# Performance work log

Hardware: AMD Instinct MI355X
Metric: run time of the kernel (lower is better)

The kernel has to match this reference:

```python
import jax, jax.numpy as jnp
import numpy as np
from jax import lax

G0, G1 = 16, 16
UNITS = 256


def setup_inputs() -> dict:
    key = jax.random.key(0)
    ks = jax.random.split(key, 20)
    B, H, W, C = 64, 512, 512, 3
    U = UNITS
    flat = 12 * 12 * 3  # after two VALID 3x3 convs on 16x16x3
    inp = {
        'image': jax.random.normal(ks[0], (B, H, W, C), jnp.float32),
        'section': jax.random.uniform(ks[1], (B, 3), jnp.float32),
        'h0': jax.random.normal(ks[2], (B, U), jnp.float32) * 0.1,
        'c0': jax.random.normal(ks[3], (B, U), jnp.float32) * 0.1,
        'conv1_k': jax.random.normal(ks[4], (3, 3, C, 3), jnp.float32) * 0.2,
        'conv1_b': jnp.zeros((3,), jnp.float32),
        'conv2_k': jax.random.normal(ks[5], (3, 3, 3, 3), jnp.float32) * 0.2,
        'conv2_b': jnp.zeros((3,), jnp.float32),
        'dense_w': jax.random.normal(ks[6], (flat, U), jnp.float32) * (1.0 / np.sqrt(flat)),
        'dense_b': jnp.zeros((U,), jnp.float32),
        'lstm_k': jax.random.normal(ks[7], (U, 4 * U), jnp.float32) * (1.0 / np.sqrt(U)),
        'lstm_rk': jax.random.normal(ks[8], (U, 4 * U), jnp.float32) * (1.0 / np.sqrt(U)),
        'lstm_b': jnp.zeros((4 * U,), jnp.float32),
        'nsc_w1': jax.random.normal(ks[9], (U, U), jnp.float32) * (1.0 / np.sqrt(U)),
        'nsc_b1': jnp.zeros((U,), jnp.float32),
        'nsc_w2': jax.random.normal(ks[10], (U, 3), jnp.float32) * (1.0 / np.sqrt(U)),
        'nsc_b2': jnp.zeros((3,), jnp.float32),
    }
    return inp


def _interpolate(image, section):
    # image: (B,H,W,C); section: (B,3) = (x, y, scale); coords in [0,1],
    # mapped linearly onto grid indices with constant (clamp) extension,
    # matching tfp.math.batch_interp_regular_nd_grid over image axes 1,2.
    B, H, W, C = image.shape
    starts = section[:, :2]                       # (B,2)
    stops = section[:, :2] + section[:, 2:]       # (B,2) broadcast scale
    t0 = jnp.linspace(0.0, 1.0, G0)               # along grid_dim[0]
    alpha = jnp.linspace(0.0, 1.0, G1)            # along grid_dim[1]
    # p0[b,i,j]: coordinate mapped to image axis 1 (H)
    p0 = (starts[:, 0, None] + t0[None, :] * (stops[:, 0] - starts[:, 0])[:, None])[:, :, None]
    p0 = jnp.broadcast_to(p0, (B, G0, G1))
    # p1[b,i,j]: coordinate mapped to image axis 2 (W)
    p1 = (starts[:, 1, None] + alpha[None, :] * (stops[:, 1] - starts[:, 1])[:, None])[:, None, :]
    p1 = jnp.broadcast_to(p1, (B, G0, G1))
    fy = jnp.clip(p0 * (H - 1), 0.0, H - 1)
    fx = jnp.clip(p1 * (W - 1), 0.0, W - 1)
    y0 = jnp.floor(fy).astype(jnp.int32)
    x0 = jnp.floor(fx).astype(jnp.int32)
    y1 = jnp.minimum(y0 + 1, H - 1)
    x1 = jnp.minimum(x0 + 1, W - 1)
    wy = (fy - y0)[..., None]
    wx = (fx - x0)[..., None]
    b = jnp.arange(B)[:, None, None]
    v00 = image[b, y0, x0]
    v01 = image[b, y0, x1]
    v10 = image[b, y1, x0]
    v11 = image[b, y1, x1]
    top = v00 * (1 - wx) + v01 * wx
    bot = v10 * (1 - wx) + v11 * wx
    return top * (1 - wy) + bot * wy            # (B,G0,G1,C)


def _conv_relu(x, k, b):
    y = lax.conv_general_dilated(x, k, (1, 1), 'VALID',
                                 dimension_numbers=('NHWC', 'HWIO', 'NHWC'))
    return jax.nn.relu(y + b)


def reference(image, section, h0, c0, conv1_k, conv1_b, conv2_k, conv2_b,
              dense_w, dense_b, lstm_k, lstm_rk, lstm_b,
              nsc_w1, nsc_b1, nsc_w2, nsc_b2):
    sec = _interpolate(image, section)                 # (B,16,16,C)
    x = _conv_relu(sec, conv1_k, conv1_b)              # (B,14,14,3)
    x = _conv_relu(x, conv2_k, conv2_b)                # (B,12,12,3)
    x = x.reshape(x.shape[0], -1)                      # (B,432)
    x = jax.nn.relu(x @ dense_w + dense_b)             # (B,U)
    # Keras LSTMCell: gate order i, f, g(c), o
    z = x @ lstm_k + h0 @ lstm_rk + lstm_b
    i, f, g, o = jnp.split(z, 4, axis=-1)
    c_new = jax.nn.sigmoid(f) * c0 + jax.nn.sigmoid(i) * jnp.tanh(g)
    h_new = jax.nn.sigmoid(o) * jnp.tanh(c_new)
    nsc = jax.nn.relu(h_new @ nsc_w1 + nsc_b1)
    next_section = jax.nn.sigmoid(nsc @ nsc_w2 + nsc_b2)  # (B,3)
    return h_new, c_new, next_section
```

## Files before the change

kernel.cpp:

```cpp
#include <hip/hip_runtime.h>
#include <math.h>

#define BATCH 64
#define IMH 512
#define IMW 512
#define UNITS 256

__device__ __forceinline__ float sigmoidf_(float x) {
    return 1.0f / (1.0f + __expf(-x));
}
__device__ __forceinline__ float tanhf_(float x) {
    float e = __expf(2.0f * x);
    return 1.0f - 2.0f / (e + 1.0f);
}

__global__ __launch_bounds__(1024) void fused_cell_kernel(
    const float* __restrict__ image,
    const float* __restrict__ section,
    const float* __restrict__ h0,
    const float* __restrict__ c0,
    const float* __restrict__ k1,
    const float* __restrict__ b1,
    const float* __restrict__ k2,
    const float* __restrict__ b2,
    const float* __restrict__ dw,
    const float* __restrict__ db,
    const float* __restrict__ lk,
    const float* __restrict__ lrk,
    const float* __restrict__ lb,
    const float* __restrict__ w1,
    const float* __restrict__ nb1,
    const float* __restrict__ w2,
    const float* __restrict__ nb2,
    float* __restrict__ out)
{
    const int b   = blockIdx.x;
    const int tid = threadIdx.x;

    __shared__ float s_sec[16][16][3];
    __shared__ float s_c1[14][14][3];
    __shared__ float s_flat[432];
    __shared__ float s_x[256];
    __shared__ float s_h0[256];
    __shared__ float s_hn[256];
    __shared__ float s_nsc[256];
    __shared__ float s_z[1024];
    __shared__ float s_part[4][256];
    __shared__ float s_k1[84];
    __shared__ float s_k2[84];

    if (tid < 81)       s_k1[tid]      = k1[tid];
    else if (tid < 84)  s_k1[tid]      = b1[tid - 81];
    else if (tid < 165) s_k2[tid - 84] = k2[tid - 84];
    else if (tid < 168) s_k2[tid - 84] = b2[tid - 165];
    if (tid < 256) s_h0[tid] = h0[b * UNITS + tid];

    if (tid < 256) {
        const float s0 = section[b * 3 + 0];
        const float s1 = section[b * 3 + 1];
        const float s2 = section[b * 3 + 2];
        const int i = tid >> 4, j = tid & 15;
        float p0 = s0 + (float)i * (1.0f / 15.0f) * s2;
        float p1 = s1 + (float)j * (1.0f / 15.0f) * s2;
        float fy = fminf(fmaxf(p0 * 511.0f, 0.0f), 511.0f);
        float fx = fminf(fmaxf(p1 * 511.0f, 0.0f), 511.0f);
        int y0 = (int)floorf(fy);
        int x0 = (int)floorf(fx);
        int y1 = min(y0 + 1, 511);
        int x1 = min(x0 + 1, 511);
        float wy = fy - (float)y0;
        float wx = fx - (float)x0;
        const float* base = image + (size_t)b * IMH * IMW * 3;
        const float* p00 = base + (y0 * IMW + x0) * 3;
        const float* p01 = base + (y0 * IMW + x1) * 3;
        const float* p10 = base + (y1 * IMW + x0) * 3;
        const float* p11 = base + (y1 * IMW + x1) * 3;
        #pragma unroll
        for (int c = 0; c < 3; ++c) {
            float top = p00[c] * (1.0f - wx) + p01[c] * wx;
            float bot = p10[c] * (1.0f - wx) + p11[c] * wx;
            s_sec[i][j][c] = top * (1.0f - wy) + bot * wy;
        }
    }
    __syncthreads();

    if (tid < 196) {
        const int i = tid / 14, j = tid % 14;
        float a0 = s_k1[81], a1 = s_k1[82], a2 = s_k1[83];
        #pragma unroll
        for (int di = 0; di < 3; ++di)
            #pragma unroll
            for (int dj = 0; dj < 3; ++dj)
                #pragma unroll
                for (int ci = 0; ci < 3; ++ci) {
                    float v = s_sec[i + di][j + dj][ci];
                    const int kb = ((di * 3 + dj) * 3 + ci) * 3;
                    a0 += v * s_k1[kb + 0];
                    a1 += v * s_k1[kb + 1];
                    a2 += v * s_k1[kb + 2];
                }
        s_c1[i][j][0] = fmaxf(a0, 0.0f);
        s_c1[i][j][1] = fmaxf(a1, 0.0f);
        s_c1[i][j][2] = fmaxf(a2, 0.0f);
    }
    __syncthreads();

    if (tid < 144) {
        const int i = tid / 12, j = tid % 12;
        float a0 = s_k2[81], a1 = s_k2[82], a2 = s_k2[83];
        #pragma unroll
        for (int di = 0; di < 3; ++di)
            #pragma unroll
            for (int dj = 0; dj < 3; ++dj)
                #pragma unroll
                for (int ci = 0; ci < 3; ++ci) {
                    float v = s_c1[i + di][j + dj][ci];
                    const int kb = ((di * 3 + dj) * 3 + ci) * 3;
                    a0 += v * s_k2[kb + 0];
                    a1 += v * s_k2[kb + 1];
                    a2 += v * s_k2[kb + 2];
                }
        const int fb = tid * 3;
        s_flat[fb + 0] = fmaxf(a0, 0.0f);
        s_flat[fb + 1] = fmaxf(a1, 0.0f);
        s_flat[fb + 2] = fmaxf(a2, 0.0f);
    }
    __syncthreads();

    {
        const int g = tid >> 8, col = tid & 255;
        const float* wp = dw + (g * 108) * 256 + col;
        const float* fp = s_flat + g * 108;
        float acc = 0.0f;
        #pragma unroll 6
        for (int k = 0; k < 108; ++k)
            acc += fp[k] * wp[k * 256];
        s_part[g][col] = acc;
    }
    __syncthreads();
    if (tid < 256)
        s_x[tid] = fmaxf(s_part[0][tid] + s_part[1][tid] + s_part[2][tid] +
                         s_part[3][tid] + db[tid], 0.0f);
    __syncthreads();

    {
        float z = lb[tid];
        const float* lkp = lk  + tid;
        const float* lrp = lrk + tid;
        #pragma unroll 8
        for (int k = 0; k < 256; ++k)
            z += s_x[k] * lkp[k * 1024] + s_h0[k] * lrp[k * 1024];
        s_z[tid] = z;
    }
    __syncthreads();
    if (tid < 256) {
        const float zi = s_z[tid];
        const float zf = s_z[256 + tid];
        const float zg = s_z[512 + tid];
        const float zo = s_z[768 + tid];
        const float cprev = c0[b * UNITS + tid];
        const float cn = sigmoidf_(zf) * cprev + sigmoidf_(zi) * tanhf_(zg);
        const float hn = sigmoidf_(zo) * tanhf_(cn);
        out[b * UNITS + tid] = hn;
        out[BATCH * UNITS + b * UNITS + tid] = cn;
        s_hn[tid] = hn;
    }
    __syncthreads();

    {
        const int g = tid >> 8, col = tid & 255;
        const float* wp = w1 + (g * 64) * 256 + col;
        const float* hp = s_hn + g * 64;
        float acc = 0.0f;
        #pragma unroll 8
        for (int k = 0; k < 64; ++k)
            acc += hp[k] * wp[k * 256];
        s_part[g][col] = acc;
    }
    __syncthreads();
    if (tid < 256)
        s_nsc[tid] = fmaxf(s_part[0][tid] + s_part[1][tid] + s_part[2][tid] +
                           s_part[3][tid] + nb1[tid], 0.0f);
    __syncthreads();

    if (tid < 192) {
        const int j = tid >> 6;
        const int l = tid & 63;
        float p = 0.0f;
        #pragma unroll
        for (int k = l; k < 256; k += 64)
            p += s_nsc[k] * w2[k * 3 + j];
        #pragma unroll
        for (int off = 32; off > 0; off >>= 1)
            p += __shfl_down(p, off);
        if (l == 0)
            out[2 * BATCH * UNITS + b * 3 + j] = sigmoidf_(p + nb2[j]);
    }
}

extern "C" void kernel_launch(void* const* d_in, const int* in_sizes, int n_in,
                              void* d_out, int out_size, void* d_ws, size_t ws_size,
                              hipStream_t stream) {
    const float* image   = (const float*)d_in[0];
    const float* section = (const float*)d_in[1];
    const float* h0      = (const float*)d_in[2];
    const float* c0      = (const float*)d_in[3];
    const float* k1      = (const float*)d_in[4];
    const float* b1      = (const float*)d_in[5];
    const float* k2      = (const float*)d_in[6];
    const float* b2      = (const float*)d_in[7];
    const float* dw      = (const float*)d_in[8];
    const float* db      = (const float*)d_in[9];
    const float* lk      = (const float*)d_in[10];
    const float* lrk     = (const float*)d_in[11];
    const float* lb      = (const float*)d_in[12];
    const float* w1      = (const float*)d_in[13];
    const float* nb1     = (const float*)d_in[14];
    const float* w2      = (const float*)d_in[15];
    const float* nb2     = (const float*)d_in[16];
    float* out = (float*)d_out;

    fused_cell_kernel<<<BATCH, 1024, 0, stream>>>(
        image, section, h0, c0, k1, b1, k2, b2, dw, db,
        lk, lrk, lb, w1, nb1, w2, nb2, out);
}
```

Before: 299.6 us.

## Vectorize matvec weight loads with float4 and split K across thread groups

The dense, LSTM and nsc matrix-vector products now have each thread load float4 weight vectors covering four output columns. The K dimension is split across more thread groups (16 for dense and nsc, 4 for LSTM), with partial sums reduced through a larger shared buffer. The goal is fewer, wider global load instructions and more memory-level parallelism per block on these bandwidth-bound weight reads. The cost is a larger shared-memory footprint (16KB partial buffer) and an extra reduction pass for the LSTM gates.

New measurement: 307.1 us. 1.02x slower.

```diff
diff --git a/kernel.cpp b/kernel.cpp
--- a/kernel.cpp
+++ b/kernel.cpp
@@ -45,7 +45,7 @@
     __shared__ float s_hn[256];
     __shared__ float s_nsc[256];
     __shared__ float s_z[1024];
-    __shared__ float s_part[4][256];
+    __shared__ float s_pf[4096];
     __shared__ float s_k1[84];
     __shared__ float s_k2[84];
 
@@ -53,7 +53,7 @@
     else if (tid < 84)  s_k1[tid]      = b1[tid - 81];
     else if (tid < 165) s_k2[tid - 84] = k2[tid - 84];
     else if (tid < 168) s_k2[tid - 84] = b2[tid - 165];
-    if (tid < 256) s_h0[tid] = h0[b * UNITS + tid];
+    if (tid >= 256 && tid < 512) s_h0[tid - 256] = h0[b * UNITS + (tid - 256)];
 
     if (tid < 256) {
         const float s0 = section[b * 3 + 0];
@@ -128,30 +128,49 @@
     __syncthreads();
 
     {
-        const int g = tid >> 8, col = tid & 255;
-        const float* wp = dw + (g * 108) * 256 + col;
-        const float* fp = s_flat + g * 108;
-        float acc = 0.0f;
-        #pragma unroll 6
-        for (int k = 0; k < 108; ++k)
-            acc += fp[k] * wp[k * 256];
-        s_part[g][col] = acc;
-    }
-    __syncthreads();
-    if (tid < 256)
-        s_x[tid] = fmaxf(s_part[0][tid] + s_part[1][tid] + s_part[2][tid] +
-                         s_part[3][tid] + db[tid], 0.0f);
+        const int g = tid >> 6, q = tid & 63;
+        const float* fp = s_flat + g * 27;
+        const float4* wp = (const float4*)(dw) + (g * 27) * 64 + q;
+        float4 acc = {0.f, 0.f, 0.f, 0.f};
+        #pragma unroll 9
+        for (int k = 0; k < 27; ++k) {
+            const float4 w = wp[k * 64];
+            const float v = fp[k];
+            acc.x += v * w.x; acc.y += v * w.y; acc.z += v * w.z; acc.w += v * w.w;
+        }
+        ((float4*)s_pf)[g * 64 + q] = acc;
+    }
+    __syncthreads();
+    if (tid < 256) {
+        float a = db[tid];
+        #pragma unroll
+        for (int g = 0; g < 16; ++g) a += s_pf[g * 256 + tid];
+        s_x[tid] = fmaxf(a, 0.0f);
+    }
     __syncthreads();
 
     {
-        float z = lb[tid];
-        const float* lkp = lk  + tid;
-        const float* lrp = lrk + tid;
+        const int g = tid >> 8, q = tid & 255;
+        const float* xk = s_x  + g * 64;
+        const float* hk = s_h0 + g * 64;
+        const float4* lkp = (const float4*)(lk)  + (g * 64) * 256 + q;
+        const float4* lrp = (const float4*)(lrk) + (g * 64) * 256 + q;
+        float4 acc = {0.f, 0.f, 0.f, 0.f};
         #pragma unroll 8
-        for (int k = 0; k < 256; ++k)
-            z += s_x[k] * lkp[k * 1024] + s_h0[k] * lrp[k * 1024];
-        s_z[tid] = z;
-    }
+        for (int k = 0; k < 64; ++k) {
+            const float4 a = lkp[k * 256];
+            const float4 r = lrp[k * 256];
+            const float xv = xk[k];
+            const float hv = hk[k];
+            acc.x += xv * a.x + hv * r.x;
+            acc.y += xv * a.y + hv * r.y;
+            acc.z += xv * a.z + hv * r.z;
+            acc.w += xv * a.w + hv * r.w;
+        }
+        ((float4*)s_pf)[g * 256 + q] = acc;
+    }
+    __syncthreads();
+    s_z[tid] = lb[tid] + s_pf[tid] + s_pf[1024 + tid] + s_pf[2048 + tid] + s_pf[3072 + tid];
     __syncthreads();
     if (tid < 256) {
         const float zi = s_z[tid];
@@ -168,19 +187,25 @@
     __syncthreads();
 
     {
-        const int g = tid >> 8, col = tid & 255;
-        const float* wp = w1 + (g * 64) * 256 + col;
-        const float* hp = s_hn + g * 64;
-        float acc = 0.0f;
-        #pragma unroll 8
-        for (int k = 0; k < 64; ++k)
-            acc += hp[k] * wp[k * 256];
-        s_part[g][col] = acc;
-    }
-    __syncthreads();
-    if (tid < 256)
-        s_nsc[tid] = fmaxf(s_part[0][tid] + s_part[1][tid] + s_part[2][tid] +
-                           s_part[3][tid] + nb1[tid], 0.0f);
+        const int g = tid >> 6, q = tid & 63;
+        const float* hp = s_hn + g * 16;
+        const float4* wp = (const float4*)(w1) + (g * 16) * 64 + q;
+        float4 acc = {0.f, 0.f, 0.f, 0.f};
+        #pragma unroll
+        for (int k = 0; k < 16; ++k) {
+            const float4 w = wp[k * 64];
+            const float v = hp[k];
+            acc.x += v * w.x; acc.y += v * w.y; acc.z += v * w.z; acc.w += v * w.w;
+        }
+        ((float4*)s_pf)[g * 64 + q] = acc;
+    }
+    __syncthreads();
+    if (tid < 256) {
+        float a = nb1[tid];
+        #pragma unroll
+        for (int g = 0; g < 16; ++g) a += s_pf[g * 256 + tid];
+        s_nsc[tid] = fmaxf(a, 0.0f);
+    }
     __syncthreads();
 
     if (tid < 192) {
```

## Split fused cell kernel into four kernels to spread LSTM GEMM across blocks

Applied to the files above, without the earlier changes.

Replaces the single 64-block fused kernel with four launches: front-end interpolation/conv/dense, a 512-block LSTM gate GEMM tiled over batch pairs and 64-column slices, a cell-update plus first NSC layer kernel, and a final NSC output kernel. Intermediates go through the workspace buffer. The aim is to use far more of the GPU's compute units for the weight-streaming GEMMs, which previously ran on only 64 blocks. The cost is extra launch overhead and global round-trips. Each LSTM weight column is also now re-read by 32 batch-pair blocks instead of 64, and the cell math is recomputed in each of the four column blocks.

Result: no change. 304.5 us (+1.6%).

```diff
diff --git a/kernel.cpp b/kernel.cpp
--- a/kernel.cpp
+++ b/kernel.cpp
@@ -14,25 +14,16 @@
     return 1.0f - 2.0f / (e + 1.0f);
 }
 
-__global__ __launch_bounds__(1024) void fused_cell_kernel(
-    const float* __restrict__ image,
-    const float* __restrict__ section,
-    const float* __restrict__ h0,
-    const float* __restrict__ c0,
-    const float* __restrict__ k1,
-    const float* __restrict__ b1,
-    const float* __restrict__ k2,
-    const float* __restrict__ b2,
-    const float* __restrict__ dw,
-    const float* __restrict__ db,
-    const float* __restrict__ lk,
-    const float* __restrict__ lrk,
-    const float* __restrict__ lb,
-    const float* __restrict__ w1,
-    const float* __restrict__ nb1,
-    const float* __restrict__ w2,
-    const float* __restrict__ nb2,
-    float* __restrict__ out)
+#define WS_X   0
+#define WS_Z   16384
+#define WS_NSC (16384 + 65536)
+
+__global__ __launch_bounds__(512) void k1_front(
+    const float* __restrict__ image, const float* __restrict__ section,
+    const float* __restrict__ k1, const float* __restrict__ b1,
+    const float* __restrict__ k2, const float* __restrict__ b2,
+    const float* __restrict__ dw, const float* __restrict__ db,
+    float* __restrict__ ws)
 {
     const int b   = blockIdx.x;
     const int tid = threadIdx.x;
@@ -40,12 +31,7 @@
     __shared__ float s_sec[16][16][3];
     __shared__ float s_c1[14][14][3];
     __shared__ float s_flat[432];
-    __shared__ float s_x[256];
-    __shared__ float s_h0[256];
-    __shared__ float s_hn[256];
-    __shared__ float s_nsc[256];
-    __shared__ float s_z[1024];
-    __shared__ float s_part[4][256];
+    __shared__ float s_part[2][256];
     __shared__ float s_k1[84];
     __shared__ float s_k2[84];
 
@@ -53,7 +39,6 @@
     else if (tid < 84)  s_k1[tid]      = b1[tid - 81];
     else if (tid < 165) s_k2[tid - 84] = k2[tid - 84];
     else if (tid < 168) s_k2[tid - 84] = b2[tid - 165];
-    if (tid < 256) s_h0[tid] = h0[b * UNITS + tid];
 
     if (tid < 256) {
         const float s0 = section[b * 3 + 0];
@@ -129,67 +114,131 @@
 
     {
         const int g = tid >> 8, col = tid & 255;
-        const float* wp = dw + (g * 108) * 256 + col;
-        const float* fp = s_flat + g * 108;
+        const int k0 = g * 216;
+        const float* fp = s_flat + k0;
+        const float* wp = dw + k0 * 256 + col;
         float acc = 0.0f;
-        #pragma unroll 6
-        for (int k = 0; k < 108; ++k)
+        #pragma unroll 8
+        for (int k = 0; k < 216; ++k)
             acc += fp[k] * wp[k * 256];
         s_part[g][col] = acc;
     }
     __syncthreads();
     if (tid < 256)
-        s_x[tid] = fmaxf(s_part[0][tid] + s_part[1][tid] + s_part[2][tid] +
-                         s_part[3][tid] + db[tid], 0.0f);
-    __syncthreads();
-
-    {
-        float z = lb[tid];
-        const float* lkp = lk  + tid;
-        const float* lrp = lrk + tid;
+        ws[WS_X + b * 256 + tid] =
+            fmaxf(s_part[0][tid] + s_part[1][tid] + db[tid], 0.0f);
+}
+
+__global__ __launch_bounds__(256) void k2_lstm_gemm(
+    const float* __restrict__ h0, const float* __restrict__ lk,
+    const float* __restrict__ lrk, const float* __restrict__ lb,
+    float* __restrict__ ws)
+{
+    const int bx   = blockIdx.x;
+    const int ct   = bx & 15;
+    const int bt   = bx >> 4;
+    const int col0 = ct * 64;
+    const int row0 = bt * 2;
+    const int tid  = threadIdx.x;
+
+    __shared__ float s_x2[2][256];
+    __shared__ float s_h2[2][256];
+    __shared__ float s_zp[2][128];
+
+    for (int i = tid; i < 512; i += 256) {
+        const int r = i >> 8, k = i & 255;
+        s_x2[r][k] = ws[WS_X + (row0 + r) * 256 + k];
+        s_h2[r][k] = h0[(row0 + r) * 256 + k];
+    }
+    __syncthreads();
+
+    {
+        const int c  = tid & 63;
+        const int b2 = (tid >> 6) & 1;
+        const int ks = tid >> 7;
+        const int k0 = ks * 128;
+        const float* lkp = lk  + (size_t)k0 * 1024 + col0 + c;
+        const float* lrp = lrk + (size_t)k0 * 1024 + col0 + c;
+        const float* xp = s_x2[b2] + k0;
+        const float* hp = s_h2[b2] + k0;
+        float acc = 0.0f;
+        #pragma unroll 8
+        for (int k = 0; k < 128; ++k)
+            acc += xp[k] * lkp[k * 1024] + hp[k] * lrp[k * 1024];
+        s_zp[ks][b2 * 64 + c] = acc;
+    }
+    __syncthreads();
+
+    if (tid < 128) {
+        const int c  = tid & 63;
+        const int b2 = tid >> 6;
+        ws[WS_Z + (row0 + b2) * 1024 + col0 + c] =
+            s_zp[0][tid] + s_zp[1][tid] + lb[col0 + c];
+    }
+}
+
+__global__ __launch_bounds__(256) void k4_cell_nsc1(
+    const float* __restrict__ c0, const float* __restrict__ w1,
+    const float* __restrict__ nb1, float* __restrict__ ws,
+    float* __restrict__ out)
+{
+    const int bx   = blockIdx.x;
+    const int ct   = bx & 3;
+    const int bt   = bx >> 2;
+    const int col0 = ct * 64;
+    const int row0 = bt * 4;
+    const int tid  = threadIdx.x;
+
+    __shared__ float s_hn[4][256];
+
+    {
+        const int u = tid;
+        #pragma unroll
+        for (int b2 = 0; b2 < 4; ++b2) {
+            const int row = row0 + b2;
+            const float zi = ws[WS_Z + row * 1024 + u];
+            const float zf = ws[WS_Z + row * 1024 + 256 + u];
+            const float zg = ws[WS_Z + row * 1024 + 512 + u];
+            const float zo = ws[WS_Z + row * 1024 + 768 + u];
+            const float cprev = c0[row * 256 + u];
+            const float cn = sigmoidf_(zf) * cprev + sigmoidf_(zi) * tanhf_(zg);
+            const float hn = sigmoidf_(zo) * tanhf_(cn);
+            s_hn[b2][u] = hn;
+            if (ct == 0) {
+                out[row * 256 + u] = hn;
+                out[BATCH * UNITS + row * 256 + u] = cn;
+            }
+        }
+    }
+    __syncthreads();
+
+    {
+        const int c   = tid & 63;
+        const int b2  = tid >> 6;
+        const int col = col0 + c;
+        const float* hp = s_hn[b2];
+        const float* wp = w1 + col;
+        float acc = nb1[col];
         #pragma unroll 8
         for (int k = 0; k < 256; ++k)
-            z += s_x[k] * lkp[k * 1024] + s_h0[k] * lrp[k * 1024];
-        s_z[tid] = z;
-    }
-    __syncthreads();
-    if (tid < 256) {
-        const float zi = s_z[tid];
-        const float zf = s_z[256 + tid];
-        const float zg = s_z[512 + tid];
-        const float zo = s_z[768 + tid];
-        const float cprev = c0[b * UNITS + tid];
-        const float cn = sigmoidf_(zf) * cprev + sigmoidf_(zi) * tanhf_(zg);
-        const float hn = sigmoidf_(zo) * tanhf_(cn);
-        out[b * UNITS + tid] = hn;
-        out[BATCH * UNITS + b * UNITS + tid] = cn;
-        s_hn[tid] = hn;
-    }
-    __syncthreads();
-
-    {
-        const int g = tid >> 8, col = tid & 255;
-        const float* wp = w1 + (g * 64) * 256 + col;
-        const float* hp = s_hn + g * 64;
-        float acc = 0.0f;
-        #pragma unroll 8
-        for (int k = 0; k < 64; ++k)
             acc += hp[k] * wp[k * 256];
-        s_part[g][col] = acc;
-    }
-    __syncthreads();
-    if (tid < 256)
-        s_nsc[tid] = fmaxf(s_part[0][tid] + s_part[1][tid] + s_part[2][tid] +
-                           s_part[3][tid] + nb1[tid], 0.0f);
-    __syncthreads();
-
+        ws[WS_NSC + (row0 + b2) * 256 + col] = fmaxf(acc, 0.0f);
+    }
+}
+
+__global__ __launch_bounds__(256) void k5_nsc2(
+    const float* __restrict__ w2, const float* __restrict__ nb2,
+    const float* __restrict__ ws, float* __restrict__ out)
+{
+    const int b   = blockIdx.x;
+    const int tid = threadIdx.x;
     if (tid < 192) {
         const int j = tid >> 6;
         const int l = tid & 63;
         float p = 0.0f;
         #pragma unroll
         for (int k = l; k < 256; k += 64)
-            p += s_nsc[k] * w2[k * 3 + j];
+            p += ws[WS_NSC + b * 256 + k] * w2[k * 3 + j];
         #pragma unroll
         for (int off = 32; off > 0; off >>= 1)
             p += __shfl_down(p, off);
@@ -219,8 +268,10 @@
     const float* w2      = (const float*)d_in[15];
     const float* nb2     = (const float*)d_in[16];
     float* out = (float*)d_out;
-
-    fused_cell_kernel<<<BATCH, 1024, 0, stream>>>(
-        image, section, h0, c0, k1, b1, k2, b2, dw, db,
-        lk, lrk, lb, w1, nb1, w2, nb2, out);
-}
+    float* ws  = (float*)d_ws;
+
+    k1_front<<<64, 512, 0, stream>>>(image, section, k1, b1, k2, b2, dw, db, ws);
+    k2_lstm_gemm<<<512, 256, 0, stream>>>(h0, lk, lrk, lb, ws);
+    k4_cell_nsc1<<<64, 256, 0, stream>>>(c0, w1, nb1, ws, out);
+    k5_nsc2<<<64, 256, 0, stream>>>(w2, nb2, ws, out);
+}
```
